# Performance work log

Hardware: AMD Instinct MI355X
Metric: run time of the kernel (lower is better)

Reference implementation:

```python
import jax, jax.numpy as jnp
import numpy as np

K = 4
KS = 7
SHIFT = KS // 2

def setup_inputs() -> dict:
    key = jax.random.key(0)
    ks = jax.random.split(key, 5)
    B, C, H, W = 8, 128, 256, 256
    x = jax.random.normal(ks[0], (B, C, H, W), dtype=jnp.float32)
    guidance = jax.random.normal(ks[1], (B, C, H, W), dtype=jnp.float32)
    basis_filters = jax.random.normal(ks[2], (K, C, KS, KS), dtype=jnp.float32)
    w1 = jax.random.normal(ks[3], (C // 4, C), dtype=jnp.float32) * (1.0 / np.sqrt(C))
    b1 = jnp.zeros((C // 4,), dtype=jnp.float32)
    w2 = jax.random.normal(ks[4], (K, C // 4), dtype=jnp.float32) * (1.0 / np.sqrt(C // 4))
    b2 = jnp.zeros((K,), dtype=jnp.float32)
    return {"x": x, "guidance": guidance, "basis_filters": basis_filters,
            "w1": w1, "b1": b1, "w2": w2, "b2": b2}

def reference(x, guidance, basis_filters, w1, b1, w2, b2):
    B, C, H, W = x.shape
    # guidance vector: global average pool -> MLP -> softmax over k bases
    g = jnp.mean(guidance, axis=(2, 3))                      # [B, C]
    h1 = jax.nn.relu(g @ w1.T + b1)                          # [B, C//4]
    weights = jax.nn.softmax(h1 @ w2.T + b2, axis=1)         # [B, K]
    # dynamic per-sample depthwise kernel: weighted sum of bases
    dyn = jnp.einsum('bk,kcij->bcij', weights, basis_filters)  # [B, C, KS, KS]
    # pad kernel to full (H, W) at the bottom/right, then roll to center at origin
    padded = jnp.pad(dyn, ((0, 0), (0, 0), (0, H - KS), (0, W - KS)))
    centered = jnp.roll(padded, shift=(-SHIFT, -SHIFT), axis=(-2, -1))
    # circular depthwise convolution via FFT
    filt_fft = jnp.fft.rfft2(centered, s=(H, W), axes=(-2, -1))
    x_fft = jnp.fft.rfft2(x, s=(H, W), axes=(-2, -1))
    out = jnp.fft.irfft2(x_fft * filt_fft, s=(H, W), axes=(-2, -1))
    return out
```

## Files before the change

### kernel.cpp

```cpp
#include <hip/hip_runtime.h>

#define HW 256
#define HWMASK 255
#define CH 128
#define BATCH 8
#define NK 4
#define STRIP 16
#define NIN (STRIP + 6)

typedef float f32x4 __attribute__((ext_vector_type(4)));

__global__ __launch_bounds__(256) void mean1_kernel(const float* __restrict__ guid,
                                                    float* __restrict__ partial) {
    int blk = blockIdx.x;
    const float4* p = (const float4*)(guid + (size_t)blk * 16384);
    float s = 0.f;
    for (int i = threadIdx.x; i < 4096; i += 256) {
        float4 v = p[i];
        s += (v.x + v.y) + (v.z + v.w);
    }
    for (int off = 32; off; off >>= 1) s += __shfl_down(s, off, 64);
    __shared__ float red[4];
    if ((threadIdx.x & 63) == 0) red[threadIdx.x >> 6] = s;
    __syncthreads();
    if (threadIdx.x == 0) partial[blk] = (red[0] + red[1]) + (red[2] + red[3]);
}

__global__ __launch_bounds__(256) void mlpdyn_kernel(const float* __restrict__ partial,
                                                     const float* __restrict__ w1,
                                                     const float* __restrict__ b1,
                                                     const float* __restrict__ w2,
                                                     const float* __restrict__ b2,
                                                     const float* __restrict__ basis,
                                                     float* __restrict__ dynF) {
    __shared__ float gs[BATCH * CH];
    __shared__ float h1[BATCH * 32];
    __shared__ float lg[BATCH * NK];
    __shared__ float wt[BATCH * NK];
    int t = threadIdx.x;
    for (int i = t; i < BATCH * CH; i += 256) {
        float4 v = *(const float4*)(partial + i * 4);
        gs[i] = ((v.x + v.y) + (v.z + v.w)) * (1.0f / 65536.0f);
    }
    __syncthreads();
    {
        int b = t >> 5, j = t & 31;
        float acc = b1[j];
        #pragma unroll 4
        for (int c = 0; c < CH; ++c) acc += gs[b * CH + c] * w1[j * CH + c];
        h1[b * 32 + j] = fmaxf(acc, 0.f);
    }
    __syncthreads();
    if (t < BATCH * NK) {
        int b = t >> 2, k = t & 3;
        float acc = b2[k];
        #pragma unroll
        for (int j = 0; j < 32; ++j) acc += h1[b * 32 + j] * w2[k * 32 + j];
        lg[b * NK + k] = acc;
    }
    __syncthreads();
    if (t < BATCH) {
        int b = t;
        float m = lg[b * 4];
        for (int k = 1; k < 4; ++k) m = fmaxf(m, lg[b * 4 + k]);
        float e[4], s = 0.f;
        for (int k = 0; k < 4; ++k) { e[k] = expf(lg[b * 4 + k] - m); s += e[k]; }
        float inv = 1.0f / s;
        for (int k = 0; k < 4; ++k) wt[b * 4 + k] = e[k] * inv;
    }
    __syncthreads();

    int idx = blockIdx.x * 256 + t;
    if (idx >= BATCH * CH * 49) return;
    int ij = idx % 49;
    int bc = idx / 49;
    int c = bc % CH;
    int b = bc / CH;
    float acc = 0.f;
    #pragma unroll
    for (int k = 0; k < NK; ++k)
        acc += wt[b * NK + k] * basis[(k * CH + c) * 49 + ij];
    dynF[bc * 49 + (48 - ij)] = acc;
}

__global__ __launch_bounds__(256) void conv_kernel(const float* __restrict__ x,
                                                   const float* __restrict__ dynF,
                                                   float* __restrict__ out) {
    int bc = blockIdx.x;
    const float* xp = x + (size_t)bc * (HW * HW);
    float* op = out + (size_t)bc * (HW * HW);
    int tid = threadIdx.x;
    int lane = tid & 63, ty = tid >> 6;
    int yb = blockIdx.y * (4 * STRIP) + ty * STRIP;

    const float* df = dynF + bc * 49;
    float d[49];
    #pragma unroll
    for (int i = 0; i < 49; ++i) d[i] = df[i];

    int col = 4 * lane;
    int lL = (lane + 63) & 63;
    int lR = (lane + 1) & 63;

    float4 pf[4];
    #pragma unroll
    for (int k = 0; k < 4; ++k)
        pf[k] = *(const float4*)(xp + (((yb + k - 3) & HWMASK) * HW) + col);

    float acc[7][4] = {};
    #pragma unroll
    for (int i = 0; i < NIN; ++i) {
        float4 Q = pf[i & 3];
        if (i + 4 < NIN)
            pf[i & 3] = *(const float4*)(xp + (((yb + i + 1) & HWMASK) * HW) + col);

        float4 L, R;
        L.x = __shfl(Q.x, lL, 64); L.y = __shfl(Q.y, lL, 64);
        L.z = __shfl(Q.z, lL, 64); L.w = __shfl(Q.w, lL, 64);
        R.x = __shfl(Q.x, lR, 64); R.y = __shfl(Q.y, lR, 64);
        R.z = __shfl(Q.z, lR, 64); R.w = __shfl(Q.w, lR, 64);
        float v[12] = {L.x, L.y, L.z, L.w, Q.x, Q.y, Q.z, Q.w, R.x, R.y, R.z, R.w};

        #pragma unroll
        for (int ii = 0; ii < 7; ++ii) {
            int o = i - ii;
            if (o >= 0 && o < STRIP) {
                const int s = ((unsigned)o) % 7;
                #pragma unroll
                for (int q = 0; q < 4; ++q) {
                    #pragma unroll
                    for (int jj = 0; jj < 7; ++jj)
                        acc[s][q] += d[ii * 7 + jj] * v[q + jj + 1];
                }
            }
        }
        if (i >= 6) {
            const int o = i - 6;
            const int s = ((unsigned)o) % 7;
            f32x4 ov = {acc[s][0], acc[s][1], acc[s][2], acc[s][3]};
            __builtin_nontemporal_store(ov, (f32x4*)(op + (yb + o) * HW + col));
            acc[s][0] = 0.f; acc[s][1] = 0.f; acc[s][2] = 0.f; acc[s][3] = 0.f;
        }
    }
}

extern "C" void kernel_launch(void* const* d_in, const int* in_sizes, int n_in,
                              void* d_out, int out_size, void* d_ws, size_t ws_size,
                              hipStream_t stream) {
    const float* x        = (const float*)d_in[0];
    const float* guidance = (const float*)d_in[1];
    const float* basis    = (const float*)d_in[2];
    const float* w1       = (const float*)d_in[3];
    const float* b1       = (const float*)d_in[4];
    const float* w2       = (const float*)d_in[5];
    const float* b2       = (const float*)d_in[6];
    float* out = (float*)d_out;
    float* ws  = (float*)d_ws;

    float* partial = ws;
    float* dynF    = ws + 4096;

    mean1_kernel<<<4096, 256, 0, stream>>>(guidance, partial);
    mlpdyn_kernel<<<(BATCH * CH * 49 + 255) / 256, 256, 0, stream>>>(partial, w1, b1, w2, b2, basis, dynF);
    conv_kernel<<<dim3(BATCH * CH, HW / (4 * STRIP)), 256, 0, stream>>>(x, dynF, out);
}
```

Measured before the change: 169.6 us.

## Fuse mean, MLP, tap build and conv into one cooperative kernel

Replaces the three-kernel pipeline with a single cooperative kernel of one block per (batch, channel). Each block reduces its guidance plane, a grid-wide sync follows, then every block redundantly runs the tiny MLP and softmax and builds its own 49 taps before doing the 7x7 circular conv over four strips. This removes two launches and the dynF round trip, at the cost of a grid barrier, redundant MLP work per block, and fewer blocks (1024 instead of 4096) for the conv stage. The old path is kept as a fallback if the cooperative launch fails.

After: 291.8 us. 1.72x slower.

```diff
diff --git a/kernel.cpp b/kernel.cpp
--- a/kernel.cpp
+++ b/kernel.cpp
@@ -1,4 +1,7 @@
 #include <hip/hip_runtime.h>
+#include <hip/hip_cooperative_groups.h>
+
+namespace cg = cooperative_groups;
 
 #define HW 256
 #define HWMASK 255
@@ -9,6 +12,144 @@
 #define NIN (STRIP + 6)
 
 typedef float f32x4 __attribute__((ext_vector_type(4)));
+
+__device__ __forceinline__ float rfl(float v) {
+    union { float f; int i; } a, b;
+    a.f = v;
+    b.i = __builtin_amdgcn_readfirstlane(a.i);
+    return b.f;
+}
+
+__global__ __launch_bounds__(256, 4) void fused_kernel(const float* __restrict__ x,
+                                                       const float* __restrict__ guid,
+                                                       const float* __restrict__ basis,
+                                                       const float* __restrict__ w1,
+                                                       const float* __restrict__ b1,
+                                                       const float* __restrict__ w2,
+                                                       const float* __restrict__ b2,
+                                                       float* __restrict__ out,
+                                                       float* __restrict__ g) {
+    int bc = blockIdx.x;
+    int tid = threadIdx.x;
+
+    {
+        const float4* p = (const float4*)(guid + (size_t)bc * (HW * HW));
+        float s = 0.f;
+        #pragma unroll 4
+        for (int i = tid; i < (HW * HW / 4); i += 256) {
+            float4 v = p[i];
+            s += (v.x + v.y) + (v.z + v.w);
+        }
+        for (int off = 32; off; off >>= 1) s += __shfl_down(s, off, 64);
+        __shared__ float red[4];
+        if ((tid & 63) == 0) red[tid >> 6] = s;
+        __syncthreads();
+        if (tid == 0)
+            atomicExch(&g[bc], ((red[0] + red[1]) + (red[2] + red[3])) * (1.0f / 65536.0f));
+    }
+    cg::this_grid().sync();
+
+    __shared__ float gs[BATCH * CH];
+    __shared__ float h1[BATCH * 32];
+    __shared__ float lg[BATCH * NK];
+    __shared__ float wts[BATCH * NK];
+    __shared__ float tap[49];
+    for (int i = tid; i < BATCH * CH; i += 256) gs[i] = g[i];
+    __syncthreads();
+    {
+        int b = tid >> 5, j = tid & 31;
+        float acc = b1[j];
+        #pragma unroll 4
+        for (int c = 0; c < CH; ++c) acc += gs[b * CH + c] * w1[j * CH + c];
+        h1[tid] = fmaxf(acc, 0.f);
+    }
+    __syncthreads();
+    if (tid < BATCH * NK) {
+        int b = tid >> 2, k = tid & 3;
+        float acc = b2[k];
+        #pragma unroll
+        for (int j = 0; j < 32; ++j) acc += h1[b * 32 + j] * w2[k * 32 + j];
+        lg[tid] = acc;
+    }
+    __syncthreads();
+    if (tid < BATCH) {
+        int b = tid;
+        float m = lg[b * 4];
+        for (int k = 1; k < 4; ++k) m = fmaxf(m, lg[b * 4 + k]);
+        float e[4], s = 0.f;
+        for (int k = 0; k < 4; ++k) { e[k] = expf(lg[b * 4 + k] - m); s += e[k]; }
+        float inv = 1.0f / s;
+        for (int k = 0; k < 4; ++k) wts[b * 4 + k] = e[k] * inv;
+    }
+    __syncthreads();
+    {
+        int b = bc >> 7, c = bc & 127;
+        if (tid < 49) {
+            float acc = 0.f;
+            #pragma unroll
+            for (int k = 0; k < NK; ++k)
+                acc += wts[b * NK + k] * basis[(k * CH + c) * 49 + tid];
+            tap[48 - tid] = acc;
+        }
+    }
+    __syncthreads();
+    float d[49];
+    #pragma unroll
+    for (int i = 0; i < 49; ++i) d[i] = rfl(tap[i]);
+
+    const float* xp = x + (size_t)bc * (HW * HW);
+    float* op = out + (size_t)bc * (HW * HW);
+    int lane = tid & 63, ty = tid >> 6;
+    int col = 4 * lane;
+    int lL = (lane + 63) & 63;
+    int lR = (lane + 1) & 63;
+
+    #pragma unroll 1
+    for (int st = 0; st < 4; ++st) {
+        int yb = 64 * ty + 16 * st;
+
+        float4 pf[4];
+        #pragma unroll
+        for (int k = 0; k < 4; ++k)
+            pf[k] = *(const float4*)(xp + (((yb + k - 3) & HWMASK) * HW) + col);
+
+        float acc[7][4] = {};
+        #pragma unroll
+        for (int i = 0; i < NIN; ++i) {
+            float4 Q = pf[i & 3];
+            if (i + 4 < NIN)
+                pf[i & 3] = *(const float4*)(xp + (((yb + i + 1) & HWMASK) * HW) + col);
+
+            float4 L, R;
+            L.x = __shfl(Q.x, lL, 64); L.y = __shfl(Q.y, lL, 64);
+            L.z = __shfl(Q.z, lL, 64); L.w = __shfl(Q.w, lL, 64);
+            R.x = __shfl(Q.x, lR, 64); R.y = __shfl(Q.y, lR, 64);
+            R.z = __shfl(Q.z, lR, 64); R.w = __shfl(Q.w, lR, 64);
+            float v[12] = {L.x, L.y, L.z, L.w, Q.x, Q.y, Q.z, Q.w, R.x, R.y, R.z, R.w};
+
+            #pragma unroll
+            for (int ii = 0; ii < 7; ++ii) {
+                int o = i - ii;
+                if (o >= 0 && o < STRIP) {
+                    const int s = ((unsigned)o) % 7;
+                    #pragma unroll
+                    for (int q = 0; q < 4; ++q) {
+                        #pragma unroll
+                        for (int jj = 0; jj < 7; ++jj)
+                            acc[s][q] += d[ii * 7 + jj] * v[q + jj + 1];
+                    }
+                }
+            }
+            if (i >= 6) {
+                const int o = i - 6;
+                const int s = ((unsigned)o) % 7;
+                f32x4 ov = {acc[s][0], acc[s][1], acc[s][2], acc[s][3]};
+                __builtin_nontemporal_store(ov, (f32x4*)(op + (yb + o) * HW + col));
+                acc[s][0] = 0.f; acc[s][1] = 0.f; acc[s][2] = 0.f; acc[s][3] = 0.f;
+            }
+        }
+    }
+}
 
 __global__ __launch_bounds__(256) void mean1_kernel(const float* __restrict__ guid,
                                                     float* __restrict__ partial) {
@@ -157,10 +298,17 @@
     float* out = (float*)d_out;
     float* ws  = (float*)d_ws;
 
-    float* partial = ws;
-    float* dynF    = ws + 4096;
-
-    mean1_kernel<<<4096, 256, 0, stream>>>(guidance, partial);
-    mlpdyn_kernel<<<(BATCH * CH * 49 + 255) / 256, 256, 0, stream>>>(partial, w1, b1, w2, b2, basis, dynF);
-    conv_kernel<<<dim3(BATCH * CH, HW / (4 * STRIP)), 256, 0, stream>>>(x, dynF, out);
-}
+    float* g = ws;
+
+    void* args[] = {(void*)&x, (void*)&guidance, (void*)&basis, (void*)&w1,
+                    (void*)&b1, (void*)&w2, (void*)&b2, (void*)&out, (void*)&g};
+    hipError_t err = hipLaunchCooperativeKernel((void*)fused_kernel, dim3(BATCH * CH),
+                                                dim3(256), args, 0, stream);
+    if (err != hipSuccess) {
+        float* partial = ws;
+        float* dynF    = ws + 4096;
+        mean1_kernel<<<4096, 256, 0, stream>>>(guidance, partial);
+        mlpdyn_kernel<<<(BATCH * CH * 49 + 255) / 256, 256, 0, stream>>>(partial, w1, b1, w2, b2, basis, dynF);
+        conv_kernel<<<dim3(BATCH * CH, HW / (4 * STRIP)), 256, 0, stream>>>(x, dynF, out);
+    }
+}
```
